# Optimization experiments

Hardware: AMD Instinct MI355X
Metric: run time of the kernel (lower is better)

Reference implementation:

```python
import jax, jax.numpy as jnp
import numpy as np

SIGMA = 1.0
EPSILON = 1.0
MAX_ITER = 10


def pairwise_kernel(x, y, sigma=SIGMA):
    # k = -||x-y||^2 / (2 sigma^2), shape [B, L, K]
    outer = jnp.einsum('bld,bkd->blk', x, y)
    nx = jnp.sum(x * x, axis=2)
    ny = jnp.sum(y * y, axis=2)
    dist = jnp.clip(nx[:, :, None] + ny[:, None, :] - 2.0 * outer, 0.0, None)
    return -dist / (2.0 * sigma ** 2)


def c_transform(potential, log_weight, kernel, epsilon=EPSILON):
    # rho=None => scale=1, lse = -eps * logsumexp(kernel/eps + (pot/eps + log_w))
    s = potential / epsilon + log_weight            # [B, K]
    operand = kernel / epsilon + s[:, None, :]      # [B, L, K]
    return -epsilon * jax.scipy.special.logsumexp(operand, axis=2)


def potentials(kxy, log_a, log_b):
    kyx = jnp.swapaxes(kxy, 1, 2)
    f0 = jnp.zeros_like(log_a)
    g0 = jnp.zeros_like(log_b)

    def step(carry, _):
        f, g = carry
        fn = c_transform(g, log_b, kxy)
        gn = c_transform(f, log_a, kyx)
        return ((fn + f) * 0.5, (gn + g) * 0.5), None

    (f, g), _ = jax.lax.scan(step, (f0, g0), None, length=MAX_ITER)
    return f, g


def sym_potential(x, log_a):
    kxx = pairwise_kernel(x, x)
    f0 = jnp.zeros_like(log_a)

    def step(f, _):
        fn = c_transform(f, log_a, kxx)
        return (fn + f) * 0.5, None

    f, _ = jax.lax.scan(step, f0, None, length=MAX_ITER)
    return f


def evaluate_potential(x, a, y, b, g):
    # phi_transform is identity for rho=None; scaled_dot_prod forward = sum(a*f, dim=1)
    kxy = pairwise_kernel(x, y)
    f = c_transform(g, jnp.log(b), kxy)
    return jnp.sum(a * f, axis=1)


def setup_inputs() -> dict:
    key = jax.random.key(0)
    k1, k2, k3, k4 = jax.random.split(key, 4)
    B, L, K, D = 8, 2048, 2048, 32
    x = jax.random.normal(k1, (B, L, D), dtype=jnp.float32)
    y = jax.random.normal(k2, (B, K, D), dtype=jnp.float32)
    a = jax.random.uniform(k3, (B, L), dtype=jnp.float32, minval=0.1, maxval=1.0)
    b = jax.random.uniform(k4, (B, K), dtype=jnp.float32, minval=0.1, maxval=1.0)
    a = a / jnp.sum(a, axis=1, keepdims=True)
    b = b / jnp.sum(b, axis=1, keepdims=True)
    return {"x": x, "a": a, "y": y, "b": b}


def reference(x, a, y, b):
    log_a, log_b = jnp.log(a), jnp.log(b)
    kxy = pairwise_kernel(x, y)
    f, g = potentials(kxy, log_a, log_b)
    dist = evaluate_potential(x, a, y, b, g) + evaluate_potential(y, b, x, a, f)
    fx = sym_potential(x, log_a)
    fy = sym_potential(y, log_b)
    ent_x = evaluate_potential(x, a, x, a, fx)
    ent_y = evaluate_potential(y, b, y, b, fy)
    return jnp.mean(dist - ent_x - ent_y)
```

## Files before the change

kernel.cpp:

```cpp
#include <hip/hip_runtime.h>
#include <math.h>

#define BATCH 8
#define NPT   2048
#define DIM   32
#define RPB   32
#define CPW   (NPT / 4)
#define NT    (CPW / 16)
#define L2E   1.44269504088896f
#define BN    (BATCH * NPT)

typedef __attribute__((ext_vector_type(8))) _Float16 half8;
typedef __attribute__((ext_vector_type(4))) float floatx4;
typedef unsigned short u16;
typedef unsigned int u32;

__device__ __forceinline__ u16 f2h_bits(float v) {
    _Float16 h = (_Float16)v;
    return *(u16*)&h;
}
__device__ __forceinline__ float exp2v(float x) { return __builtin_amdgcn_exp2f(x); }

struct CtSet {
    const u16* Ah;
    const u16* Bh;
    const float* tls;
    const float* qX;
    const float* bmIn;
    const float* cwNext;
    const float* prev;
    float* out;
    float* tlsOut;
    float* bmOut;
};
struct CtArgs { CtSet s[4]; int average; };

__global__ __launch_bounds__(256, 8) void ct_kernel(CtArgs args) {
    const CtSet cs = args.s[blockIdx.y];
    const int batch = blockIdx.z;
    const int row0 = blockIdx.x * RPB;
    const int tid  = threadIdx.x;
    const int w = tid >> 6, lane = tid & 63, n = lane & 15, quad = lane >> 4;
    const int qk = quad * 8;
    const size_t pbase = (size_t)batch * NPT * DIM;
    const size_t vbase = (size_t)batch * NPT;

    __shared__ float lsum[RPB][4];

    const u16* __restrict__ Ah = cs.Ah + pbase;
    const u16* __restrict__ Bh = cs.Bh + pbase;
    const float* __restrict__ tls = cs.tls + vbase;

    half8 ah[2];
    #pragma unroll
    for (int s = 0; s < 2; s++) {
        size_t off = (size_t)(row0 + s * 16 + n) * DIM + qk;
        ah[s] = *(const half8*)(Ah + off);
    }

    float tmv = fmaxf(cs.bmIn[batch * 128 + lane], cs.bmIn[batch * 128 + 64 + lane]);
    #pragma unroll
    for (int m = 1; m < 64; m <<= 1) tmv = fmaxf(tmv, __shfl_xor(tmv, m, 64));
    const float Tmax = tmv;
    const float l2eTmax = L2E * Tmax;

    float sum[2][4];
    #pragma unroll
    for (int s = 0; s < 2; s++)
        #pragma unroll
        for (int r = 0; r < 4; r++) sum[s][r] = 0.0f;

    const int c0 = w * CPW + n;
    const u16* bp = Bh + (size_t)c0 * DIM + qk;
    const float* tp = tls + c0;

    half8 b0, b1;
    float t0, t1;
    b0 = *(const half8*)bp;  t0 = *tp;

    #pragma unroll 1
    for (int ch = 0; ch < NT; ch += 2) {
        b1 = *(const half8*)(bp + (size_t)(ch + 1) * 16 * DIM);
        t1 = tp[(ch + 1) * 16];
        {
            float wq = exp2v(t0 - l2eTmax);
            floatx4 acc[2];
            #pragma unroll
            for (int s = 0; s < 2; s++) acc[s] = (floatx4){0.f, 0.f, 0.f, 0.f};
            #pragma unroll
            for (int s = 0; s < 2; s++)
                acc[s] = __builtin_amdgcn_mfma_f32_16x16x32_f16(ah[s], b0, acc[s], 0, 0, 0);
            #pragma unroll
            for (int s = 0; s < 2; s++)
                #pragma unroll
                for (int r = 0; r < 4; r++)
                    sum[s][r] = fmaf(wq, exp2v(acc[s][r]), sum[s][r]);
        }
        if (ch + 2 < NT) {
            b0 = *(const half8*)(bp + (size_t)(ch + 2) * 16 * DIM);
            t0 = tp[(ch + 2) * 16];
        }
        {
            float wq = exp2v(t1 - l2eTmax);
            floatx4 acc[2];
            #pragma unroll
            for (int s = 0; s < 2; s++) acc[s] = (floatx4){0.f, 0.f, 0.f, 0.f};
            #pragma unroll
            for (int s = 0; s < 2; s++)
                acc[s] = __builtin_amdgcn_mfma_f32_16x16x32_f16(ah[s], b1, acc[s], 0, 0, 0);
            #pragma unroll
            for (int s = 0; s < 2; s++)
                #pragma unroll
                for (int r = 0; r < 4; r++)
                    sum[s][r] = fmaf(wq, exp2v(acc[s][r]), sum[s][r]);
        }
    }

    #pragma unroll
    for (int s = 0; s < 2; s++)
        #pragma unroll
        for (int r = 0; r < 4; r++) {
            float v = sum[s][r];
            #pragma unroll
            for (int m = 1; m < 16; m <<= 1) v += __shfl_xor(v, m, 64);
            if (n == 0) lsum[s * 16 + quad * 4 + r][w] = v;
        }
    __syncthreads();

    if (tid < RPB) {
        float T = (lsum[tid][0] + lsum[tid][1]) + (lsum[tid][2] + lsum[tid][3]);
        int l = row0 + tid;
        float lse = Tmax + __logf(T);
        float val = cs.qX[vbase + l] - lse;
        if (args.average) val = 0.5f * (cs.prev[vbase + l] + val);
        cs.out[vbase + l] = val;
        float tc = val + cs.cwNext[vbase + l];
        cs.tlsOut[vbase + l] = L2E * tc;
        float bm = tc;
        #pragma unroll
        for (int m = 1; m < 16; m <<= 1) bm = fmaxf(bm, __shfl_xor(bm, m, 64));
        if ((tid & 15) == 0)
            cs.bmOut[batch * 128 + blockIdx.x * 2 + (tid >> 4)] = bm;
    }
}

struct InitArgs {
    const float *x, *a, *y, *b;
    float *c_x, *c_y, *qx, *qy;
    u16 *xh, *yh, *xsh, *ysh;
    float *f0, *g0, *fx0, *fy0;
    float *tlsF0, *tlsG0, *tlsFx0, *tlsFy0;
    float *bmF0, *bmG0, *bmFx0, *bmFy0;
};

__global__ __launch_bounds__(256) void init_kernel(InitArgs ia) {
    int idx = blockIdx.x * 256 + threadIdx.x;
    if (idx >= BN) return;
    const float* xp = ia.x + (size_t)idx * DIM;
    const float* yp = ia.y + (size_t)idx * DIM;
    u32* xhp  = (u32*)ia.xh  + (size_t)idx * (DIM / 2);
    u32* yhp  = (u32*)ia.yh  + (size_t)idx * (DIM / 2);
    u32* xshp = (u32*)ia.xsh + (size_t)idx * (DIM / 2);
    u32* yshp = (u32*)ia.ysh + (size_t)idx * (DIM / 2);
    float sx = 0.f, sy = 0.f;
    #pragma unroll
    for (int d = 0; d < DIM; d += 2) {
        float v0 = xp[d], v1 = xp[d + 1];
        sx += v0 * v0 + v1 * v1;
        xhp[d / 2]  = (u32)f2h_bits(v0) | ((u32)f2h_bits(v1) << 16);
        xshp[d / 2] = (u32)f2h_bits(L2E * v0) | ((u32)f2h_bits(L2E * v1) << 16);
        float u0 = yp[d], u1 = yp[d + 1];
        sy += u0 * u0 + u1 * u1;
        yhp[d / 2]  = (u32)f2h_bits(u0) | ((u32)f2h_bits(u1) << 16);
        yshp[d / 2] = (u32)f2h_bits(L2E * u0) | ((u32)f2h_bits(L2E * u1) << 16);
    }
    float qxv = 0.5f * sx, qyv = 0.5f * sy;
    ia.qx[idx] = qxv; ia.qy[idx] = qyv;
    float cxv = __logf(ia.a[idx]) - qxv;
    float cyv = __logf(ia.b[idx]) - qyv;
    ia.c_x[idx] = cxv; ia.c_y[idx] = cyv;
    ia.f0[idx] = 0.f; ia.g0[idx] = 0.f; ia.fx0[idx] = 0.f; ia.fy0[idx] = 0.f;
    ia.tlsF0[idx] = L2E * cxv; ia.tlsG0[idx] = L2E * cyv;
    ia.tlsFx0[idx] = L2E * cxv; ia.tlsFy0[idx] = L2E * cyv;
    float mx = cxv, my = cyv;
    #pragma unroll
    for (int m = 1; m < 16; m <<= 1) {
        mx = fmaxf(mx, __shfl_xor(mx, m, 32));
        my = fmaxf(my, __shfl_xor(my, m, 32));
    }
    if ((threadIdx.x & 15) == 0) {
        int g = idx >> 4;
        ia.bmF0[g] = mx; ia.bmFx0[g] = mx;
        ia.bmG0[g] = my; ia.bmFy0[g] = my;
    }
}

__global__ __launch_bounds__(1024) void reduce_kernel(
        const float* __restrict__ a, const float* __restrict__ b,
        const float* __restrict__ ctA, const float* __restrict__ ctB,
        const float* __restrict__ ctX, const float* __restrict__ ctY,
        float* __restrict__ out) {
    float acc = 0.f;
    for (int idx = threadIdx.x; idx < BN; idx += 1024) {
        acc += a[idx] * (ctA[idx] - ctX[idx]) + b[idx] * (ctB[idx] - ctY[idx]);
    }
    #pragma unroll
    for (int off = 32; off > 0; off >>= 1) acc += __shfl_down(acc, off, 64);
    __shared__ float sm[16];
    if ((threadIdx.x & 63) == 0) sm[threadIdx.x >> 6] = acc;
    __syncthreads();
    if (threadIdx.x == 0) {
        float t = 0.f;
        #pragma unroll
        for (int i = 0; i < 16; i++) t += sm[i];
        out[0] = t / (float)BATCH;
    }
}

extern "C" void kernel_launch(void* const* d_in, const int* in_sizes, int n_in,
                              void* d_out, int out_size, void* d_ws, size_t ws_size,
                              hipStream_t stream) {
    const float* x = (const float*)d_in[0];
    const float* a = (const float*)d_in[1];
    const float* y = (const float*)d_in[2];
    const float* b = (const float*)d_in[3];
    float* out = (float*)d_out;

    float* ws = (float*)d_ws;
    float* c_x = ws + 0 * BN;
    float* c_y = ws + 1 * BN;
    float* qx  = ws + 2 * BN;
    float* qy  = ws + 3 * BN;
    float* fb[2]  = { ws + 4 * BN,  ws + 5 * BN };
    float* gb[2]  = { ws + 6 * BN,  ws + 7 * BN };
    float* fxb[2] = { ws + 8 * BN,  ws + 9 * BN };
    float* fyb[2] = { ws + 10 * BN, ws + 11 * BN };
    float* ctA = ws + 12 * BN;
    float* ctB = ws + 13 * BN;
    float* ctX = ws + 14 * BN;
    float* ctY = ws + 15 * BN;
    float* tlsF[2]  = { ws + 16 * BN, ws + 17 * BN };
    float* tlsG[2]  = { ws + 18 * BN, ws + 19 * BN };
    float* tlsFx[2] = { ws + 20 * BN, ws + 21 * BN };
    float* tlsFy[2] = { ws + 22 * BN, ws + 23 * BN };
    float* dummyT = ws + 24 * BN;
    float* small = ws + 25 * BN;
    float* bmF[2]  = { small + 0 * 1024, small + 1 * 1024 };
    float* bmG[2]  = { small + 2 * 1024, small + 3 * 1024 };
    float* bmFx[2] = { small + 4 * 1024, small + 5 * 1024 };
    float* bmFy[2] = { small + 6 * 1024, small + 7 * 1024 };
    float* dummyB = small + 8 * 1024;
    u16* bf = (u16*)(small + 10 * 1024);
    const size_t AS = (size_t)BN * DIM;
    u16* xh  = bf + 0 * AS;
    u16* yh  = bf + 1 * AS;
    u16* xsh = bf + 2 * AS;
    u16* ysh = bf + 3 * AS;

    InitArgs ia;
    ia.x = x; ia.a = a; ia.y = y; ia.b = b;
    ia.c_x = c_x; ia.c_y = c_y; ia.qx = qx; ia.qy = qy;
    ia.xh = xh; ia.yh = yh; ia.xsh = xsh; ia.ysh = ysh;
    ia.f0 = fb[0]; ia.g0 = gb[0]; ia.fx0 = fxb[0]; ia.fy0 = fyb[0];
    ia.tlsF0 = tlsF[0]; ia.tlsG0 = tlsG[0]; ia.tlsFx0 = tlsFx[0]; ia.tlsFy0 = tlsFy[0];
    ia.bmF0 = bmF[0]; ia.bmG0 = bmG[0]; ia.bmFx0 = bmFx[0]; ia.bmFy0 = bmFy[0];
    init_kernel<<<BN / 256, 256, 0, stream>>>(ia);

    dim3 grid(NPT / RPB, 4, BATCH);
    int cur = 0;
    for (int it = 0; it < 10; it++) {
        CtArgs ar;
        ar.average = 1;
        ar.s[0] = { xh, ysh, tlsG[cur], qx, bmG[cur], c_x,
                    fb[cur], fb[1 - cur], tlsF[1 - cur], bmF[1 - cur] };
        ar.s[1] = { yh, xsh, tlsF[cur], qy, bmF[cur], c_y,
                    gb[cur], gb[1 - cur], tlsG[1 - cur], bmG[1 - cur] };
        ar.s[2] = { xh, xsh, tlsFx[cur], qx, bmFx[cur], c_x,
                    fxb[cur], fxb[1 - cur], tlsFx[1 - cur], bmFx[1 - cur] };
        ar.s[3] = { yh, ysh, tlsFy[cur], qy, bmFy[cur], c_y,
                    fyb[cur], fyb[1 - cur], tlsFy[1 - cur], bmFy[1 - cur] };
        ct_kernel<<<grid, 256, 0, stream>>>(ar);
        cur ^= 1;
    }

    CtArgs fin;
    fin.average = 0;
    fin.s[0] = { xh, ysh, tlsG[cur], qx, bmG[cur], c_x, fb[cur], ctA, dummyT, dummyB };
    fin.s[1] = { yh, xsh, tlsF[cur], qy, bmF[cur], c_y, gb[cur], ctB, dummyT, dummyB };
    fin.s[2] = { xh, xsh, tlsFx[cur], qx, bmFx[cur], c_x, fxb[cur], ctX, dummyT, dummyB };
    fin.s[3] = { yh, ysh, tlsFy[cur], qy, bmFy[cur], c_y, fyb[cur], ctY, dummyT, dummyB };
    ct_kernel<<<grid, 256, 0, stream>>>(fin);

    reduce_kernel<<<1, 1024, 0, stream>>>(a, b, ctA, ctB, ctX, ctY, out);
}
```

Before: 329.0 us.

## Compute f and g c-transforms from one shared x·y kernel pass

The f-update block now computes exp of the x·y kernel once and uses each tile for both the row sums (f) and weighted column partial sums (g), writing per-block column partials to a workspace. A new gfin kernel reduces those partials into g, which removes the separate y·x c-transform pass and cuts the MFMA and exp work for the cross term roughly in half. The symmetric passes also fold the bias into the MFMA accumulator initialisation, dropping a per-tile exp and multiply. The cost is an extra kernel launch per iteration, extra global traffic for the partial-sum buffer, and fewer waves per SIMD (launch bound 7 instead of 8) because the fused path needs more registers.

```diff
diff --git a/kernel.cpp b/kernel.cpp
--- a/kernel.cpp
+++ b/kernel.cpp
@@ -7,6 +7,7 @@
 #define RPB   32
 #define CPW   (NPT / 4)
 #define NT    (CPW / 16)
+#define NBLK  (NPT / RPB)
 #define L2E   1.44269504088896f
 #define BN    (BATCH * NPT)
 
@@ -21,7 +22,7 @@
 }
 __device__ __forceinline__ float exp2v(float x) { return __builtin_amdgcn_exp2f(x); }
 
-struct CtSet {
+struct SymSet {
     const u16* Ah;
     const u16* Bh;
     const float* tls;
@@ -33,10 +34,24 @@
     float* tlsOut;
     float* bmOut;
 };
-struct CtArgs { CtSet s[4]; int average; };
-
-__global__ __launch_bounds__(256, 8) void ct_kernel(CtArgs args) {
-    const CtSet cs = args.s[blockIdx.y];
+struct FusedSet {
+    const u16* Xh;
+    const u16* Ysh;
+    const float* tlsG;
+    const float* tlsF;
+    const float* qX;
+    const float* bmG;
+    const float* bmF;
+    const float* c_x;
+    const float* prevF;
+    float* outF;
+    float* tlsFOut;
+    float* bmFOut;
+    float* gpart;
+};
+struct CtArgs { FusedSet fs; SymSet s[2]; int average; };
+
+__global__ __launch_bounds__(256, 7) void ct2_kernel(CtArgs args) {
     const int batch = blockIdx.z;
     const int row0 = blockIdx.x * RPB;
     const int tid  = threadIdx.x;
@@ -47,101 +62,245 @@
 
     __shared__ float lsum[RPB][4];
 
-    const u16* __restrict__ Ah = cs.Ah + pbase;
-    const u16* __restrict__ Bh = cs.Bh + pbase;
-    const float* __restrict__ tls = cs.tls + vbase;
-
-    half8 ah[2];
-    #pragma unroll
-    for (int s = 0; s < 2; s++) {
-        size_t off = (size_t)(row0 + s * 16 + n) * DIM + qk;
-        ah[s] = *(const half8*)(Ah + off);
-    }
-
-    float tmv = fmaxf(cs.bmIn[batch * 128 + lane], cs.bmIn[batch * 128 + 64 + lane]);
-    #pragma unroll
-    for (int m = 1; m < 64; m <<= 1) tmv = fmaxf(tmv, __shfl_xor(tmv, m, 64));
-    const float Tmax = tmv;
-    const float l2eTmax = L2E * Tmax;
-
-    float sum[2][4];
-    #pragma unroll
-    for (int s = 0; s < 2; s++)
-        #pragma unroll
-        for (int r = 0; r < 4; r++) sum[s][r] = 0.0f;
-
-    const int c0 = w * CPW + n;
-    const u16* bp = Bh + (size_t)c0 * DIM + qk;
-    const float* tp = tls + c0;
-
-    half8 b0, b1;
-    float t0, t1;
-    b0 = *(const half8*)bp;  t0 = *tp;
-
-    #pragma unroll 1
-    for (int ch = 0; ch < NT; ch += 2) {
-        b1 = *(const half8*)(bp + (size_t)(ch + 1) * 16 * DIM);
-        t1 = tp[(ch + 1) * 16];
-        {
-            float wq = exp2v(t0 - l2eTmax);
+    if (blockIdx.y == 0) {
+        const FusedSet fs = args.fs;
+        const u16* __restrict__ Ah = fs.Xh + pbase;
+        const u16* __restrict__ Bh = fs.Ysh + pbase;
+        const float* __restrict__ tg = fs.tlsG + vbase;
+        const float* __restrict__ tf = fs.tlsF + vbase;
+
+        half8 ah[2];
+        #pragma unroll
+        for (int s = 0; s < 2; s++) {
+            size_t off = (size_t)(row0 + s * 16 + n) * DIM + qk;
+            ah[s] = *(const half8*)(Ah + off);
+        }
+
+        float mg = fmaxf(fs.bmG[batch * 128 + lane], fs.bmG[batch * 128 + 64 + lane]);
+        float mf = fmaxf(fs.bmF[batch * 128 + lane], fs.bmF[batch * 128 + 64 + lane]);
+        #pragma unroll
+        for (int m = 1; m < 64; m <<= 1) {
+            mg = fmaxf(mg, __shfl_xor(mg, m, 64));
+            mf = fmaxf(mf, __shfl_xor(mf, m, 64));
+        }
+        const float TmaxG = mg;
+        const float l2eTG = L2E * mg, l2eTF = L2E * mf;
+
+        float vw[2][4];
+        #pragma unroll
+        for (int s = 0; s < 2; s++)
+            #pragma unroll
+            for (int r = 0; r < 4; r++)
+                vw[s][r] = exp2v(tf[row0 + s * 16 + quad * 4 + r] - l2eTF);
+
+        float sumF[2][4];
+        #pragma unroll
+        for (int s = 0; s < 2; s++)
+            #pragma unroll
+            for (int r = 0; r < 4; r++) sumF[s][r] = 0.0f;
+
+        const int c0 = w * CPW + n;
+        const u16* bp = Bh + (size_t)c0 * DIM + qk;
+        const float* tp = tg + c0;
+        float* gpc = fs.gpart + ((size_t)batch * NBLK + blockIdx.x) * NPT + c0;
+
+        half8 b0, b1;
+        float t0, t1;
+        b0 = *(const half8*)bp;  t0 = *tp;
+
+        auto tile = [&](half8 b, float t, int idx) {
+            float wq = exp2v(t - l2eTG);
             floatx4 acc[2];
             #pragma unroll
             for (int s = 0; s < 2; s++) acc[s] = (floatx4){0.f, 0.f, 0.f, 0.f};
             #pragma unroll
             for (int s = 0; s < 2; s++)
-                acc[s] = __builtin_amdgcn_mfma_f32_16x16x32_f16(ah[s], b0, acc[s], 0, 0, 0);
+                acc[s] = __builtin_amdgcn_mfma_f32_16x16x32_f16(ah[s], b, acc[s], 0, 0, 0);
+            float gl = 0.0f;
+            #pragma unroll
+            for (int s = 0; s < 2; s++)
+                #pragma unroll
+                for (int r = 0; r < 4; r++) {
+                    float e = exp2v(acc[s][r]);
+                    sumF[s][r] = fmaf(wq, e, sumF[s][r]);
+                    gl = fmaf(vw[s][r], e, gl);
+                }
+            gl += __shfl_xor(gl, 16, 64);
+            gl += __shfl_xor(gl, 32, 64);
+            if (lane < 16) gpc[idx * 16] = gl;
+        };
+
+        #pragma unroll 1
+        for (int ch = 0; ch < NT; ch += 2) {
+            b1 = *(const half8*)(bp + (size_t)(ch + 1) * 16 * DIM);
+            t1 = tp[(ch + 1) * 16];
+            tile(b0, t0, ch);
+            if (ch + 2 < NT) {
+                b0 = *(const half8*)(bp + (size_t)(ch + 2) * 16 * DIM);
+                t0 = tp[(ch + 2) * 16];
+            }
+            tile(b1, t1, ch + 1);
+        }
+
+        #pragma unroll
+        for (int s = 0; s < 2; s++)
+            #pragma unroll
+            for (int r = 0; r < 4; r++) {
+                float v = sumF[s][r];
+                #pragma unroll
+                for (int m = 1; m < 16; m <<= 1) v += __shfl_xor(v, m, 64);
+                if (n == 0) lsum[s * 16 + quad * 4 + r][w] = v;
+            }
+        __syncthreads();
+
+        if (tid < RPB) {
+            float T = (lsum[tid][0] + lsum[tid][1]) + (lsum[tid][2] + lsum[tid][3]);
+            int l = row0 + tid;
+            float lse = TmaxG + __logf(T);
+            float val = fs.qX[vbase + l] - lse;
+            if (args.average) val = 0.5f * (fs.prevF[vbase + l] + val);
+            fs.outF[vbase + l] = val;
+            float tc = val + fs.c_x[vbase + l];
+            fs.tlsFOut[vbase + l] = L2E * tc;
+            float bm = tc;
+            #pragma unroll
+            for (int m = 1; m < 16; m <<= 1) bm = fmaxf(bm, __shfl_xor(bm, m, 64));
+            if ((tid & 15) == 0)
+                fs.bmFOut[batch * 128 + blockIdx.x * 2 + (tid >> 4)] = bm;
+        }
+    } else {
+        const SymSet cs = args.s[blockIdx.y - 1];
+        const u16* __restrict__ Ah = cs.Ah + pbase;
+        const u16* __restrict__ Bh = cs.Bh + pbase;
+        const float* __restrict__ tls = cs.tls + vbase;
+
+        half8 ah[2];
+        #pragma unroll
+        for (int s = 0; s < 2; s++) {
+            size_t off = (size_t)(row0 + s * 16 + n) * DIM + qk;
+            ah[s] = *(const half8*)(Ah + off);
+        }
+
+        float tmv = fmaxf(cs.bmIn[batch * 128 + lane], cs.bmIn[batch * 128 + 64 + lane]);
+        #pragma unroll
+        for (int m = 1; m < 64; m <<= 1) tmv = fmaxf(tmv, __shfl_xor(tmv, m, 64));
+        const float Tmax = tmv;
+        const float l2eTmax = L2E * Tmax;
+
+        float sum[2][4];
+        #pragma unroll
+        for (int s = 0; s < 2; s++)
+            #pragma unroll
+            for (int r = 0; r < 4; r++) sum[s][r] = 0.0f;
+
+        const int c0 = w * CPW + n;
+        const u16* bp = Bh + (size_t)c0 * DIM + qk;
+        const float* tp = tls + c0;
+
+        half8 b0, b1;
+        float t0, t1;
+        b0 = *(const half8*)bp;  t0 = *tp;
+
+        auto tile = [&](half8 b, float t) {
+            float bias = t - l2eTmax;
+            floatx4 ci = (floatx4){bias, bias, bias, bias};
+            floatx4 acc[2];
+            #pragma unroll
+            for (int s = 0; s < 2; s++)
+                acc[s] = __builtin_amdgcn_mfma_f32_16x16x32_f16(ah[s], b, ci, 0, 0, 0);
             #pragma unroll
             for (int s = 0; s < 2; s++)
                 #pragma unroll
                 for (int r = 0; r < 4; r++)
-                    sum[s][r] = fmaf(wq, exp2v(acc[s][r]), sum[s][r]);
-        }
-        if (ch + 2 < NT) {
-            b0 = *(const half8*)(bp + (size_t)(ch + 2) * 16 * DIM);
-            t0 = tp[(ch + 2) * 16];
-        }
-        {
-            float wq = exp2v(t1 - l2eTmax);
-            floatx4 acc[2];
-            #pragma unroll
-            for (int s = 0; s < 2; s++) acc[s] = (floatx4){0.f, 0.f, 0.f, 0.f};
-            #pragma unroll
-            for (int s = 0; s < 2; s++)
-                acc[s] = __builtin_amdgcn_mfma_f32_16x16x32_f16(ah[s], b1, acc[s], 0, 0, 0);
-            #pragma unroll
-            for (int s = 0; s < 2; s++)
+                    sum[s][r] += exp2v(acc[s][r]);
+        };
+
+        #pragma unroll 1
+        for (int ch = 0; ch < NT; ch += 2) {
+            b1 = *(const half8*)(bp + (size_t)(ch + 1) * 16 * DIM);
+            t1 = tp[(ch + 1) * 16];
+            tile(b0, t0);
+            if (ch + 2 < NT) {
+                b0 = *(const half8*)(bp + (size_t)(ch + 2) * 16 * DIM);
+                t0 = tp[(ch + 2) * 16];
+            }
+            tile(b1, t1);
+        }
+
+        #pragma unroll
+        for (int s = 0; s < 2; s++)
+            #pragma unroll
+            for (int r = 0; r < 4; r++) {
+                float v = sum[s][r];
                 #pragma unroll
-                for (int r = 0; r < 4; r++)
-                    sum[s][r] = fmaf(wq, exp2v(acc[s][r]), sum[s][r]);
-        }
-    }
-
+                for (int m = 1; m < 16; m <<= 1) v += __shfl_xor(v, m, 64);
+                if (n == 0) lsum[s * 16 + quad * 4 + r][w] = v;
+            }
+        __syncthreads();
+
+        if (tid < RPB) {
+            float T = (lsum[tid][0] + lsum[tid][1]) + (lsum[tid][2] + lsum[tid][3]);
+            int l = row0 + tid;
+            float lse = Tmax + __logf(T);
+            float val = cs.qX[vbase + l] - lse;
+            if (args.average) val = 0.5f * (cs.prev[vbase + l] + val);
+            cs.out[vbase + l] = val;
+            float tc = val + cs.cwNext[vbase + l];
+            cs.tlsOut[vbase + l] = L2E * tc;
+            float bm = tc;
+            #pragma unroll
+            for (int m = 1; m < 16; m <<= 1) bm = fmaxf(bm, __shfl_xor(bm, m, 64));
+            if ((tid & 15) == 0)
+                cs.bmOut[batch * 128 + blockIdx.x * 2 + (tid >> 4)] = bm;
+        }
+    }
+}
+
+struct GfArgs {
+    const float* gpart;
+    const float* bmF;
+    const float* qY;
+    const float* prevG;
+    const float* c_y;
+    float* outG;
+    float* tlsGOut;
+    float* bmGOut;
+    int average;
+};
+
+__global__ __launch_bounds__(256) void gfin_kernel(GfArgs a) {
+    const int tid = threadIdx.x;
+    const int bx  = blockIdx.x;
+    const int batch = bx >> 3;
+    const int col = (bx & 7) * 256 + tid;
+
+    __shared__ float sb[128];
+    if (tid < 128) sb[tid] = a.bmF[batch * 128 + tid];
+    __syncthreads();
+    if (tid < 64) {
+        float m = fmaxf(sb[tid], sb[tid + 64]);
+        #pragma unroll
+        for (int k = 1; k < 64; k <<= 1) m = fmaxf(m, __shfl_xor(m, k, 64));
+        if (tid == 0) sb[0] = m;
+    }
+    __syncthreads();
+    const float Tmax = sb[0];
+
+    const float* gp = a.gpart + (size_t)batch * NBLK * NPT + col;
+    float G = 0.0f;
+    #pragma unroll 4
+    for (int p = 0; p < NBLK; p++) G += gp[(size_t)p * NPT];
+
+    const size_t idx = (size_t)batch * NPT + col;
+    float val = a.qY[idx] - (Tmax + __logf(G));
+    if (a.average) val = 0.5f * (a.prevG[idx] + val);
+    a.outG[idx] = val;
+    float tc = val + a.c_y[idx];
+    a.tlsGOut[idx] = L2E * tc;
+    float bm = tc;
     #pragma unroll
-    for (int s = 0; s < 2; s++)
-        #pragma unroll
-        for (int r = 0; r < 4; r++) {
-            float v = sum[s][r];
-            #pragma unroll
-            for (int m = 1; m < 16; m <<= 1) v += __shfl_xor(v, m, 64);
-            if (n == 0) lsum[s * 16 + quad * 4 + r][w] = v;
-        }
-    __syncthreads();
-
-    if (tid < RPB) {
-        float T = (lsum[tid][0] + lsum[tid][1]) + (lsum[tid][2] + lsum[tid][3]);
-        int l = row0 + tid;
-        float lse = Tmax + __logf(T);
-        float val = cs.qX[vbase + l] - lse;
-        if (args.average) val = 0.5f * (cs.prev[vbase + l] + val);
-        cs.out[vbase + l] = val;
-        float tc = val + cs.cwNext[vbase + l];
-        cs.tlsOut[vbase + l] = L2E * tc;
-        float bm = tc;
-        #pragma unroll
-        for (int m = 1; m < 16; m <<= 1) bm = fmaxf(bm, __shfl_xor(bm, m, 64));
-        if ((tid & 15) == 0)
-            cs.bmOut[batch * 128 + blockIdx.x * 2 + (tid >> 4)] = bm;
-    }
+    for (int m = 1; m < 16; m <<= 1) bm = fmaxf(bm, __shfl_xor(bm, m, 64));
+    if ((tid & 15) == 0) a.bmGOut[batch * 128 + (col >> 4)] = bm;
 }
 
 struct InitArgs {
@@ -256,6 +415,7 @@
     u16* yh  = bf + 1 * AS;
     u16* xsh = bf + 2 * AS;
     u16* ysh = bf + 3 * AS;
+    float* gpart = (float*)(bf + 4 * AS);
 
     InitArgs ia;
     ia.x = x; ia.a = a; ia.y = y; ia.b = b;
@@ -266,30 +426,35 @@
     ia.bmF0 = bmF[0]; ia.bmG0 = bmG[0]; ia.bmFx0 = bmFx[0]; ia.bmFy0 = bmFy[0];
     init_kernel<<<BN / 256, 256, 0, stream>>>(ia);
 
-    dim3 grid(NPT / RPB, 4, BATCH);
+    dim3 grid(NBLK, 3, BATCH);
     int cur = 0;
     for (int it = 0; it < 10; it++) {
         CtArgs ar;
         ar.average = 1;
-        ar.s[0] = { xh, ysh, tlsG[cur], qx, bmG[cur], c_x,
-                    fb[cur], fb[1 - cur], tlsF[1 - cur], bmF[1 - cur] };
-        ar.s[1] = { yh, xsh, tlsF[cur], qy, bmF[cur], c_y,
-                    gb[cur], gb[1 - cur], tlsG[1 - cur], bmG[1 - cur] };
-        ar.s[2] = { xh, xsh, tlsFx[cur], qx, bmFx[cur], c_x,
+        ar.fs = { xh, ysh, tlsG[cur], tlsF[cur], qx, bmG[cur], bmF[cur], c_x,
+                  fb[cur], fb[1 - cur], tlsF[1 - cur], bmF[1 - cur], gpart };
+        ar.s[0] = { xh, xsh, tlsFx[cur], qx, bmFx[cur], c_x,
                     fxb[cur], fxb[1 - cur], tlsFx[1 - cur], bmFx[1 - cur] };
-        ar.s[3] = { yh, ysh, tlsFy[cur], qy, bmFy[cur], c_y,
+        ar.s[1] = { yh, ysh, tlsFy[cur], qy, bmFy[cur], c_y,
                     fyb[cur], fyb[1 - cur], tlsFy[1 - cur], bmFy[1 - cur] };
-        ct_kernel<<<grid, 256, 0, stream>>>(ar);
+        ct2_kernel<<<grid, 256, 0, stream>>>(ar);
+
+        GfArgs ga = { gpart, bmF[cur], qy, gb[cur], c_y,
+                      gb[1 - cur], tlsG[1 - cur], bmG[1 - cur], 1 };
+        gfin_kernel<<<64, 256, 0, stream>>>(ga);
         cur ^= 1;
     }
 
     CtArgs fin;
     fin.average = 0;
-    fin.s[0] = { xh, ysh, tlsG[cur], qx, bmG[cur], c_x, fb[cur], ctA, dummyT, dummyB };
-    fin.s[1] = { yh, xsh, tlsF[cur], qy, bmF[cur], c_y, gb[cur], ctB, dummyT, dummyB };
-    fin.s[2] = { xh, xsh, tlsFx[cur], qx, bmFx[cur], c_x, fxb[cur], ctX, dummyT, dummyB };
-    fin.s[3] = { yh, ysh, tlsFy[cur], qy, bmFy[cur], c_y, fyb[cur], ctY, dummyT, dummyB };
-    ct_kernel<<<grid, 256, 0, stream>>>(fin);
+    fin.fs = { xh, ysh, tlsG[cur], tlsF[cur], qx, bmG[cur], bmF[cur], c_x,
+               fb[cur], ctA, dummyT, dummyB, gpart };
+    fin.s[0] = { xh, xsh, tlsFx[cur], qx, bmFx[cur], c_x, fxb[cur], ctX, dummyT, dummyB };
+    fin.s[1] = { yh, ysh, tlsFy[cur], qy, bmFy[cur], c_y, fyb[cur], ctY, dummyT, dummyB };
+    ct2_kernel<<<grid, 256, 0, stream>>>(fin);
+
+    GfArgs gf = { gpart, bmF[cur], qy, gb[cur], c_y, ctB, dummyT, dummyB, 0 };
+    gfin_kernel<<<64, 256, 0, stream>>>(gf);
 
     reduce_kernel<<<1, 1024, 0, stream>>>(a, b, ctA, ctB, ctX, ctY, out);
 }
```

Result: slower. 416.4 us (+26.6%).
